# Kernel optimization log

Hardware: AMD Instinct MI355X
Metric: run time of the kernel (lower is better)

The kernel has to match this reference:

```python
import jax, jax.numpy as jnp
import numpy as np

VOC = 32000
D = 512          # embedding_dim == hidden_dim
POS = 1024       # position_embeddings_count


def _layernorm(x, gamma, beta, eps=1e-5):
    mu = jnp.mean(x, axis=-1, keepdims=True)
    var = jnp.var(x, axis=-1, keepdims=True)
    return (x - mu) * jax.lax.rsqrt(var + eps) * gamma + beta


def setup_inputs() -> dict:
    key = jax.random.key(0)
    ks = jax.random.split(key, 7)
    inp = jax.random.randint(ks[0], (32, 1024), 0, VOC)
    word_emb = jax.random.normal(ks[1], (VOC, D), dtype=jnp.float32) * 0.02
    pos_emb = jax.random.normal(ks[2], (POS, D), dtype=jnp.float32) * 0.02
    gamma = jnp.ones((D,), dtype=jnp.float32)
    beta = jnp.zeros((D,), dtype=jnp.float32)
    # torch.rand -> uniform [0,1) init in the original Attention module
    Wk = jax.random.uniform(ks[3], (D, D), dtype=jnp.float32)
    Wq = jax.random.uniform(ks[4], (D, D), dtype=jnp.float32)
    Wv = jax.random.uniform(ks[5], (D, D), dtype=jnp.float32)
    return {"input": inp, "word_emb": word_emb, "pos_emb": pos_emb,
            "gamma": gamma, "beta": beta, "Wk": Wk, "Wq": Wq, "Wv": Wv}


def reference(input, word_emb, pos_emb, gamma, beta, Wk, Wq, Wv):
    S = input.shape[-1]
    # MiniBertEmbedding: word + positional, then LayerNorm
    emb = word_emb[input] + pos_emb[:S][None, :, :]   # [B,S,D]
    x = _layernorm(emb, gamma, beta)
    # Attention: single-head QK^T softmax V with param matrices
    k = jnp.einsum('bsd,dh->bsh', x, Wk)
    q = jnp.einsum('bsd,dh->bsh', x, Wq)
    v = jnp.einsum('bsd,do->bso', x, Wv)
    qk = jnp.einsum('bqh,bkh->bqk', q, k) / jnp.sqrt(jnp.float32(D))
    attn = jax.nn.softmax(qk, axis=-1)
    return jnp.einsum('bqk,bko->bqo', attn, v)
```

## Files before the change

kernel.cpp:

```cpp
#include <hip/hip_runtime.h>
#include <math.h>

typedef _Float16 f16;
typedef _Float16 half8 __attribute__((ext_vector_type(8)));
typedef _Float16 hv2 __attribute__((ext_vector_type(2)));
typedef _Float16 hv4 __attribute__((ext_vector_type(4)));
typedef float f32x4 __attribute__((ext_vector_type(4)));
typedef __attribute__((address_space(1))) const unsigned int gu32;
typedef __attribute__((address_space(3))) unsigned int lu32;

#define BB 32
#define SS 1024
#define DD 512
#define NR (BB*SS)
#define CH 16

__device__ __forceinline__ void stage128(const char* g, int ldb, char* lds,
                                         int wv, int ln) {
  #pragma unroll
  for (int r = 0; r < 4; r++) {
    int slot = r * 256 + wv * 64 + ln;
    int row = slot >> 3, cp = slot & 7;
    int c = cp ^ (row & 7);
    const char* gp = g + (size_t)row * ldb + (c << 4);
    char* lp = lds + ((slot - ln) << 4);
    __builtin_amdgcn_global_load_lds((gu32*)gp, (lu32*)lp, 16, 0, 0);
  }
}

__device__ __forceinline__ void stage8k_512(const char* g, int ldb, char* lds) {
  int tid = threadIdx.x;
  int slot = tid;
  int row = slot >> 3, cp = slot & 7;
  int c = cp ^ (row & 7);
  const char* gp = g + (size_t)row * ldb + (c << 4);
  char* lp = lds + ((slot - (tid & 63)) << 4);
  __builtin_amdgcn_global_load_lds((gu32*)gp, (lu32*)lp, 16, 0, 0);
}

__device__ __forceinline__ half8 frag_ld(const char* lds, int row, int kc) {
  return *(const half8*)(lds + row * 128 + ((kc ^ (row & 7)) << 4));
}

__device__ __forceinline__ f32x4 MF(half8 a, half8 b, f32x4 c) {
  return __builtin_amdgcn_mfma_f32_16x16x32_f16(a, b, c, 0, 0, 0);
}

__global__ __launch_bounds__(256) void k_prep(
    const int* __restrict__ inp, const float* __restrict__ wemb,
    const float* __restrict__ pemb, const float* __restrict__ gamma,
    const float* __restrict__ beta, f16* __restrict__ Xhi, f16* __restrict__ Xlo,
    const float* __restrict__ Wq, const float* __restrict__ Wk,
    const float* __restrict__ Wv, f16* __restrict__ Wqh, f16* __restrict__ Wql,
    f16* __restrict__ Wkh, f16* __restrict__ Wkl, f16* __restrict__ Wvt)
{
  int bid = blockIdx.x;
  int tid = threadIdx.x;
  __shared__ float red[10];
  __shared__ float Lt[64][65];
  if (bid >= NR) {
    int t  = bid - NR;
    int mz = t >> 6;
    int tt = t & 63;
    if (mz < 2) {
      const float* W = mz ? Wk : Wq;
      f16* Oh = mz ? Wkh : Wqh;
      f16* Ol = mz ? Wkl : Wql;
      #pragma unroll
      for (int p = 0; p < 4; p++) {
        size_t base = (size_t)tt * 4096 + p * 1024 + tid * 4;
        float4 v = *(const float4*)&W[base];
        f16 h0 = (f16)v.x, h1 = (f16)v.y, h2 = (f16)v.z, h3 = (f16)v.w;
        hv4 hi = {h0, h1, h2, h3};
        hv4 lo = {(f16)(v.x - (float)h0), (f16)(v.y - (float)h1),
                  (f16)(v.z - (float)h2), (f16)(v.w - (float)h3)};
        *(hv4*)&Oh[base] = hi;
        *(hv4*)&Ol[base] = lo;
      }
      return;
    }
    int tr = tt >> 3, tc = tt & 7;
    int rr = tid >> 4;
    int c4 = (tid & 15) * 4;
    #pragma unroll
    for (int p = 0; p < 4; p++) {
      float4 v = *(const float4*)&Wv[(size_t)(tr * 64 + p * 16 + rr) * DD + tc * 64 + c4];
      Lt[p * 16 + rr][c4 + 0] = v.x; Lt[p * 16 + rr][c4 + 1] = v.y;
      Lt[p * 16 + rr][c4 + 2] = v.z; Lt[p * 16 + rr][c4 + 3] = v.w;
    }
    __syncthreads();
    #pragma unroll
    for (int p = 0; p < 4; p++) {
      int dl = p * 16 + rr;
      float v0 = Lt[c4 + 0][dl], v1 = Lt[c4 + 1][dl];
      float v2 = Lt[c4 + 2][dl], v3 = Lt[c4 + 3][dl];
      size_t o = (size_t)(tc * 64 + dl) * DD + tr * 64 + c4;
      *(hv4*)&Wvt[o] = (hv4){(f16)v0, (f16)v1, (f16)v2, (f16)v3};
    }
    return;
  }
  int row = bid;
  int s   = row & (SS - 1);
  int tok = inp[row];
  float2 w = ((const float2*)(wemb + (size_t)tok * DD))[tid];
  float2 p = ((const float2*)(pemb + (size_t)s   * DD))[tid];
  float ex = w.x + p.x, ey = w.y + p.y;
  float sum = ex + ey, ssq = ex*ex + ey*ey;
  #pragma unroll
  for (int off = 32; off > 0; off >>= 1) {
    sum += __shfl_down(sum, off, 64);
    ssq += __shfl_down(ssq, off, 64);
  }
  int wv = tid >> 6, ln = tid & 63;
  if (ln == 0) { red[wv] = sum; red[4 + wv] = ssq; }
  __syncthreads();
  if (tid == 0) {
    float s4 = red[0] + red[1] + red[2] + red[3];
    float q4 = red[4] + red[5] + red[6] + red[7];
    float mean = s4 * (1.0f / DD);
    float var  = q4 * (1.0f / DD) - mean * mean;
    red[8] = mean; red[9] = rsqrtf(var + 1e-5f);
  }
  __syncthreads();
  float mean = red[8], rstd = red[9];
  float2 g  = ((const float2*)gamma)[tid];
  float2 bt = ((const float2*)beta)[tid];
  float ox = (ex - mean) * rstd * g.x + bt.x;
  float oy = (ey - mean) * rstd * g.y + bt.y;
  f16 hx = (f16)ox, hy = (f16)oy;
  f16 lx = (f16)(ox - (float)hx), ly = (f16)(oy - (float)hy);
  ((hv2*)(Xhi + (size_t)row * DD))[tid] = (hv2){hx, hy};
  ((hv2*)(Xlo + (size_t)row * DD))[tid] = (hv2){lx, ly};
}

__global__ __launch_bounds__(256, 2) void k_mt(
    const f16* __restrict__ Wkh, const f16* __restrict__ Wkl,
    const f16* __restrict__ Wqh, const f16* __restrict__ Wql,
    f16* __restrict__ Mthi, f16* __restrict__ Mtlo)
{
  __shared__ __align__(16) char Ah[16384], Al[16384], Bh[16384], Bl[16384];
  int tid = threadIdx.x, wv = tid >> 6, ln = tid & 63;
  int mw = wv & 1, nw = wv >> 1;
  int n0 = blockIdx.x * 128;
  int m0 = blockIdx.y * 128;
  f32x4 acc[4][4];
  #pragma unroll
  for (int i = 0; i < 4; i++)
    #pragma unroll
    for (int j = 0; j < 4; j++) acc[i][j] = (f32x4)(0.0f);
  int quad = ln >> 4, l15 = ln & 15;
  for (int k0 = 0; k0 < DD; k0 += 64) {
    __syncthreads();
    stage128((const char*)(Wkh + (size_t)m0 * DD + k0), 1024, Ah, wv, ln);
    stage128((const char*)(Wkl + (size_t)m0 * DD + k0), 1024, Al, wv, ln);
    stage128((const char*)(Wqh + (size_t)n0 * DD + k0), 1024, Bh, wv, ln);
    stage128((const char*)(Wql + (size_t)n0 * DD + k0), 1024, Bl, wv, ln);
    __syncthreads();
    #pragma unroll
    for (int ks = 0; ks < 2; ks++) {
      int kc = ks * 4 + quad;
      half8 ah[4], al[4], bh[4], bl[4];
      #pragma unroll
      for (int t = 0; t < 4; t++) {
        ah[t] = frag_ld(Ah, mw * 64 + t * 16 + l15, kc);
        al[t] = frag_ld(Al, mw * 64 + t * 16 + l15, kc);
        bh[t] = frag_ld(Bh, nw * 64 + t * 16 + l15, kc);
        bl[t] = frag_ld(Bl, nw * 64 + t * 16 + l15, kc);
      }
      #pragma unroll
      for (int i = 0; i < 4; i++)
        #pragma unroll
        for (int j = 0; j < 4; j++) {
          acc[i][j] = MF(ah[i], bh[j], acc[i][j]);
          acc[i][j] = MF(ah[i], bl[j], acc[i][j]);
          acc[i][j] = MF(al[i], bh[j], acc[i][j]);
        }
    }
  }
  #pragma unroll
  for (int i = 0; i < 4; i++)
    #pragma unroll
    for (int j = 0; j < 4; j++)
      #pragma unroll
      for (int rg = 0; rg < 4; rg++) {
        int gm = m0 + mw * 64 + i * 16 + quad * 4 + rg;
        int gn = n0 + nw * 64 + j * 16 + l15;
        size_t o = (size_t)gm * DD + gn;
        float v = acc[i][j][rg];
        f16 h = (f16)v;
        Mthi[o] = h; Mtlo[o] = (f16)(v - (float)h);
      }
}

__global__ __launch_bounds__(256, 2) void k_projm(
    const f16* __restrict__ Xhi, const f16* __restrict__ Xlo,
    const f16* __restrict__ Mthi, const f16* __restrict__ Mtlo,
    f16* __restrict__ Sqhi, f16* __restrict__ Sqlo)
{
  __shared__ __align__(16) char Ah[16384], Al[16384], Bh[16384], Bl[16384];
  int tid = threadIdx.x, wv = tid >> 6, ln = tid & 63;
  int mw = wv & 1, nw = wv >> 1;
  int L = blockIdx.x;
  int xb = (L >> 3) & 3;
  int y  = ((L >> 5) << 3) + (L & 7);
  int n0 = xb * 128;
  int m0 = y * 128;
  f32x4 acc[4][4];
  #pragma unroll
  for (int i = 0; i < 4; i++)
    #pragma unroll
    for (int j = 0; j < 4; j++) acc[i][j] = (f32x4)(0.0f);
  int quad = ln >> 4, l15 = ln & 15;
  for (int k0 = 0; k0 < DD; k0 += 64) {
    __syncthreads();
    stage128((const char*)(Xhi  + (size_t)m0 * DD + k0), 1024, Ah, wv, ln);
    stage128((const char*)(Xlo  + (size_t)m0 * DD + k0), 1024, Al, wv, ln);
    stage128((const char*)(Mthi + (size_t)n0 * DD + k0), 1024, Bh, wv, ln);
    stage128((const char*)(Mtlo + (size_t)n0 * DD + k0), 1024, Bl, wv, ln);
    __syncthreads();
    #pragma unroll
    for (int ks = 0; ks < 2; ks++) {
      int kc = ks * 4 + quad;
      half8 ah[4], al[4], bh[4], bl[4];
      #pragma unroll
      for (int t = 0; t < 4; t++) {
        ah[t] = frag_ld(Ah, mw * 64 + t * 16 + l15, kc);
        al[t] = frag_ld(Al, mw * 64 + t * 16 + l15, kc);
        bh[t] = frag_ld(Bh, nw * 64 + t * 16 + l15, kc);
        bl[t] = frag_ld(Bl, nw * 64 + t * 16 + l15, kc);
      }
      #pragma unroll
      for (int i = 0; i < 4; i++)
        #pragma unroll
        for (int j = 0; j < 4; j++) {
          acc[i][j] = MF(ah[i], bh[j], acc[i][j]);
          acc[i][j] = MF(ah[i], bl[j], acc[i][j]);
          acc[i][j] = MF(al[i], bh[j], acc[i][j]);
        }
    }
  }
  #pragma unroll
  for (int i = 0; i < 4; i++)
    #pragma unroll
    for (int j = 0; j < 4; j++)
      #pragma unroll
      for (int rg = 0; rg < 4; rg++) {
        int gm = m0 + mw * 64 + i * 16 + quad * 4 + rg;
        int gn = n0 + nw * 64 + j * 16 + l15;
        size_t o = (size_t)gm * DD + gn;
        float v = acc[i][j][rg];
        f16 h = (f16)v;
        Sqhi[o] = h; Sqlo[o] = (f16)(v - (float)h);
      }
}

__global__ __launch_bounds__(256, 2) void k_vt(
    const f16* __restrict__ Wvt, const f16* __restrict__ Xhi, f16* __restrict__ Vt)
{
  __shared__ __align__(16) char Ah[2][16384], Bh[2][16384];
  int tid = threadIdx.x, wv = tid >> 6, ln = tid & 63;
  int mw = wv & 1, nw = wv >> 1;
  int orig = blockIdx.x;
  int L = (orig & 7) * 128 + (orig >> 3);
  int c = L >> 7, t = L & 127;
  int m0 = (t & 3) * 128;
  int n0 = (c * 32 + (t >> 2)) * 128;
  f32x4 acc[4][4];
  #pragma unroll
  for (int i = 0; i < 4; i++)
    #pragma unroll
    for (int j = 0; j < 4; j++) acc[i][j] = (f32x4)(0.0f);
  int quad = ln >> 4, l15 = ln & 15;
  stage128((const char*)(Wvt + (size_t)m0 * DD), 1024, Ah[0], wv, ln);
  stage128((const char*)(Xhi + (size_t)n0 * DD), 1024, Bh[0], wv, ln);
  for (int k0 = 0; k0 < DD; k0 += 64) {
    int cur = (k0 >> 6) & 1;
    __builtin_amdgcn_s_barrier();
    __builtin_amdgcn_sched_barrier(0);
    if (k0 + 64 < DD) {
      stage128((const char*)(Wvt + (size_t)m0 * DD + k0 + 64), 1024, Ah[cur ^ 1], wv, ln);
      stage128((const char*)(Xhi + (size_t)n0 * DD + k0 + 64), 1024, Bh[cur ^ 1], wv, ln);
      asm volatile("s_waitcnt vmcnt(8)" ::: "memory");
    } else {
      asm volatile("s_waitcnt vmcnt(0)" ::: "memory");
    }
    __builtin_amdgcn_s_barrier();
    __builtin_amdgcn_sched_barrier(0);
    #pragma unroll
    for (int ks = 0; ks < 2; ks++) {
      int kc = ks * 4 + quad;
      half8 a[4], b[4];
      #pragma unroll
      for (int tt = 0; tt < 4; tt++) {
        a[tt] = frag_ld(Ah[cur], mw * 64 + tt * 16 + l15, kc);
        b[tt] = frag_ld(Bh[cur], nw * 64 + tt * 16 + l15, kc);
      }
      #pragma unroll
      for (int i = 0; i < 4; i++)
        #pragma unroll
        for (int j = 0; j < 4; j++) acc[i][j] = MF(a[i], b[j], acc[i][j]);
    }
  }
  #pragma unroll
  for (int i = 0; i < 4; i++)
    #pragma unroll
    for (int j = 0; j < 4; j++)
      #pragma unroll
      for (int rg = 0; rg < 4; rg++) {
        int gm = m0 + mw * 64 + i * 16 + quad * 4 + rg;
        int gn = n0 + nw * 64 + j * 16 + l15;
        Vt[(size_t)gm * NR + gn] = (f16)acc[i][j][rg];
      }
}

__global__ __launch_bounds__(512, 2) void k_qk(
    const f16* __restrict__ Sqhi, const f16* __restrict__ Sqlo,
    const f16* __restrict__ Xhi, const f16* __restrict__ Xlo,
    f16* __restrict__ Pws, f16* __restrict__ Pd)
{
  __shared__ __align__(16) char Ah[8192], Al[8192];
  __shared__ __align__(16) char Bh[2][4][8192], Bl[2][4][8192];
  __shared__ float redm[4][64], reds[4][64];
  int tid = threadIdx.x, wv = tid >> 6, ln = tid & 63;
  int rowg = wv & 1, qd = wv >> 1;
  int L = blockIdx.x;
  int g  = L >> 7;
  int rr = L & 127;
  int z  = g * 8 + (rr & 7);
  int m0 = (rr >> 3) * 64;
  size_t zr = (size_t)z * SS;
  f32x4 acc[2][16];
  #pragma unroll
  for (int i = 0; i < 2; i++)
    #pragma unroll
    for (int j = 0; j < 16; j++) acc[i][j] = (f32x4)(0.0f);
  int quad = ln >> 4, l15 = ln & 15;

  #pragma unroll
  for (int q4 = 0; q4 < 4; q4++) {
    stage8k_512((const char*)(Xhi + (zr + q4 * 256) * DD), 1024, Bh[0][q4]);
    stage8k_512((const char*)(Xlo + (zr + q4 * 256) * DD), 1024, Bl[0][q4]);
  }

  half8 afh[2][2], afl[2][2];
  for (int k0 = 0; k0 < DD; k0 += 64) {
    #pragma unroll
    for (int r = 0; r < 4; r++) {
      __builtin_amdgcn_s_barrier();
      __builtin_amdgcn_sched_barrier(0);
      if (r == 0) {
        stage8k_512((const char*)(Sqhi + (zr + m0) * DD + k0), 1024, Ah);
        stage8k_512((const char*)(Sqlo + (zr + m0) * DD + k0), 1024, Al);
      }
      bool haveNext = !(k0 == DD - 64 && r == 3);
      if (haveNext) {
        int nk0 = (r == 3) ? k0 + 64 : k0;
        int nr  = (r + 1) & 3;
        #pragma unroll
        for (int q4 = 0; q4 < 4; q4++) {
          int n0 = q4 * 256 + nr * 64;
          stage8k_512((const char*)(Xhi + (zr + n0) * DD + nk0), 1024, Bh[(r + 1) & 1][q4]);
          stage8k_512((const char*)(Xlo + (zr + n0) * DD + nk0), 1024, Bl[(r + 1) & 1][q4]);
        }
        asm volatile("s_waitcnt vmcnt(8)" ::: "memory");
      } else {
        asm volatile("s_waitcnt vmcnt(0)" ::: "memory");
      }
      __builtin_amdgcn_s_barrier();
      __builtin_amdgcn_sched_barrier(0);
      if (r == 0) {
        #pragma unroll
        for (int ks = 0; ks < 2; ks++)
          #pragma unroll
          for (int i = 0; i < 2; i++) {
            afh[ks][i] = frag_ld(Ah, rowg * 32 + i * 16 + l15, ks * 4 + quad);
            afl[ks][i] = frag_ld(Al, rowg * 32 + i * 16 + l15, ks * 4 + quad);
          }
      }
      #pragma unroll
      for (int ks = 0; ks < 2; ks++) {
        int kc = ks * 4 + quad;
        #pragma unroll
        for (int jj = 0; jj < 4; jj++) {
          half8 bh = frag_ld(Bh[r & 1][qd], jj * 16 + l15, kc);
          half8 bl = frag_ld(Bl[r & 1][qd], jj * 16 + l15, kc);
          #pragma unroll
          for (int i = 0; i < 2; i++) {
            acc[i][r * 4 + jj] = MF(afh[ks][i], bh, acc[i][r * 4 + jj]);
            acc[i][r * 4 + jj] = MF(afh[ks][i], bl, acc[i][r * 4 + jj]);
            acc[i][r * 4 + jj] = MF(afl[ks][i], bh, acc[i][r * 4 + jj]);
          }
        }
      }
    }
  }

  const float scale = 0.044194173824159216f;
  float mx[2][4];
  #pragma unroll
  for (int i = 0; i < 2; i++)
    #pragma unroll
    for (int rg = 0; rg < 4; rg++) mx[i][rg] = -3.0e38f;
  #pragma unroll
  for (int i = 0; i < 2; i++)
    #pragma unroll
    for (int j = 0; j < 16; j++)
      #pragma unroll
      for (int rg = 0; rg < 4; rg++) {
        acc[i][j][rg] *= scale;
        mx[i][rg] = fmaxf(mx[i][rg], acc[i][j][rg]);
      }
  #pragma unroll
  for (int off = 1; off < 16; off <<= 1)
    #pragma unroll
    for (int i = 0; i < 2; i++)
      #pragma unroll
      for (int rg = 0; rg < 4; rg++)
        mx[i][rg] = fmaxf(mx[i][rg], __shfl_xor(mx[i][rg], off, 64));
  if (l15 == 0) {
    #pragma unroll
    for (int i = 0; i < 2; i++)
      #pragma unroll
      for (int rg = 0; rg < 4; rg++)
        redm[qd][rowg * 32 + i * 16 + quad * 4 + rg] = mx[i][rg];
  }
  __syncthreads();
  float fm[2][4], sum[2][4];
  #pragma unroll
  for (int i = 0; i < 2; i++)
    #pragma unroll
    for (int rg = 0; rg < 4; rg++) {
      int row = rowg * 32 + i * 16 + quad * 4 + rg;
      fm[i][rg] = fmaxf(fmaxf(redm[0][row], redm[1][row]),
                        fmaxf(redm[2][row], redm[3][row]));
      sum[i][rg] = 0.0f;
    }
  #pragma unroll
  for (int i = 0; i < 2; i++)
    #pragma unroll
    for (int j = 0; j < 16; j++)
      #pragma unroll
      for (int rg = 0; rg < 4; rg++) {
        float e = __expf(acc[i][j][rg] - fm[i][rg]);
        acc[i][j][rg] = e;
        sum[i][rg] += e;
      }
  #pragma unroll
  for (int off = 1; off < 16; off <<= 1)
    #pragma unroll
    for (int i = 0; i < 2; i++)
      #pragma unroll
      for (int rg = 0; rg < 4; rg++)
        sum[i][rg] += __shfl_xor(sum[i][rg], off, 64);
  if (l15 == 0) {
    #pragma unroll
    for (int i = 0; i < 2; i++)
      #pragma unroll
      for (int rg = 0; rg < 4; rg++)
        reds[qd][rowg * 32 + i * 16 + quad * 4 + rg] = sum[i][rg];
  }
  __syncthreads();
  float inv[2][4];
  #pragma unroll
  for (int i = 0; i < 2; i++)
    #pragma unroll
    for (int rg = 0; rg < 4; rg++) {
      int row = rowg * 32 + i * 16 + quad * 4 + rg;
      inv[i][rg] = 1.0f / (reds[0][row] + reds[1][row] + reds[2][row] + reds[3][row]);
    }
  f16* Pb = (z < CH) ? Pws : Pd;
  size_t zo = (size_t)((z < CH) ? z : z - CH);
  #pragma unroll
  for (int i = 0; i < 2; i++)
    #pragma unroll
    for (int j = 0; j < 16; j++)
      #pragma unroll
      for (int rg = 0; rg < 4; rg++) {
        int row = rowg * 32 + i * 16 + quad * 4 + rg;
        int col = qd * 256 + j * 16 + l15;
        Pb[(zo * SS + m0 + row) * SS + col] = (f16)(acc[i][j][rg] * inv[i][rg]);
      }
}

__global__ __launch_bounds__(256, 2) void k_pv(
    const f16* __restrict__ P, const f16* __restrict__ Vt, float* __restrict__ O,
    int zoff)
{
  __shared__ __align__(16) char Ah[2][16384], Bh[2][16384];
  int tid = threadIdx.x, wv = tid >> 6, ln = tid & 63;
  int mw = wv & 1, nw = wv >> 1;
  int orig = blockIdx.x;
  int L = (orig & 7) * 64 + (orig >> 3);
  int c = L >> 6, t = L & 63;
  int zl = 2 * c + (t >> 5);
  int m0 = ((t >> 2) & 7) * 128;
  int n0 = (t & 3) * 128;
  int b  = zoff + zl;
  const char* Pt = (const char*)(P + ((size_t)zl * SS + m0) * SS);
  const char* Vb = (const char*)(Vt + (size_t)n0 * NR + (size_t)b * SS);
  f32x4 acc[4][4];
  #pragma unroll
  for (int i = 0; i < 4; i++)
    #pragma unroll
    for (int j = 0; j < 4; j++) acc[i][j] = (f32x4)(0.0f);
  int quad = ln >> 4, l15 = ln & 15;
  stage128(Pt, 2048, Ah[0], wv, ln);
  stage128(Vb, NR * 2, Bh[0], wv, ln);
  for (int k0 = 0; k0 < SS; k0 += 64) {
    int cur = (k0 >> 6) & 1;
    __builtin_amdgcn_s_barrier();
    __builtin_amdgcn_sched_barrier(0);
    if (k0 + 64 < SS) {
      stage128(Pt + (k0 + 64) * 2, 2048, Ah[cur ^ 1], wv, ln);
      stage128(Vb + (k0 + 64) * 2, NR * 2, Bh[cur ^ 1], wv, ln);
      asm volatile("s_waitcnt vmcnt(8)" ::: "memory");
    } else {
      asm volatile("s_waitcnt vmcnt(0)" ::: "memory");
    }
    __builtin_amdgcn_s_barrier();
    __builtin_amdgcn_sched_barrier(0);
    #pragma unroll
    for (int ks = 0; ks < 2; ks++) {
      int kc = ks * 4 + quad;
      half8 a[4], bf[4];
      #pragma unroll
      for (int tt = 0; tt < 4; tt++) {
        a[tt]  = frag_ld(Ah[cur], mw * 64 + tt * 16 + l15, kc);
        bf[tt] = frag_ld(Bh[cur], nw * 64 + tt * 16 + l15, kc);
      }
      #pragma unroll
      for (int i = 0; i < 4; i++)
        #pragma unroll
        for (int j = 0; j < 4; j++) acc[i][j] = MF(a[i], bf[j], acc[i][j]);
    }
  }
  #pragma unroll
  for (int i = 0; i < 4; i++)
    #pragma unroll
    for (int j = 0; j < 4; j++)
      #pragma unroll
      for (int rg = 0; rg < 4; rg++) {
        int gm = m0 + mw * 64 + i * 16 + quad * 4 + rg;
        int gn = n0 + nw * 64 + j * 16 + l15;
        O[((size_t)b * SS + gm) * DD + gn] = acc[i][j][rg];
      }
}

extern "C" void kernel_launch(void* const* d_in, const int* in_sizes, int n_in,
                              void* d_out, int out_size, void* d_ws, size_t ws_size,
                              hipStream_t stream) {
  const int*   inp   = (const int*)d_in[0];
  const float* wemb  = (const float*)d_in[1];
  const float* pemb  = (const float*)d_in[2];
  const float* gamma = (const float*)d_in[3];
  const float* beta  = (const float*)d_in[4];
  const float* Wk    = (const float*)d_in[5];
  const float* Wq    = (const float*)d_in[6];
  const float* Wv    = (const float*)d_in[7];

  char* ws = (char*)d_ws;
  f16* Xhi  = (f16*)ws;
  f16* Xlo  = (f16*)(ws + ((size_t)32 << 20));
  f16* Sqhi = (f16*)(ws + ((size_t)64 << 20));
  f16* Sqlo = (f16*)(ws + ((size_t)96 << 20));
  f16* Vt   = (f16*)(ws + ((size_t)128 << 20));
  f16* Pws  = (f16*)(ws + ((size_t)160 << 20));
  f16* Pd   = (f16*)d_out;

  f16* Wqh  = (f16*)d_out;
  f16* Wql  = Wqh + (size_t)DD * DD;
  f16* Wkh  = Wql + (size_t)DD * DD;
  f16* Wkl  = Wkh + (size_t)DD * DD;
  f16* Wvt  = Wkl + (size_t)DD * DD;
  f16* Mthi = Wvt + (size_t)DD * DD;
  f16* Mtlo = Mthi + (size_t)DD * DD;

  k_prep<<<NR + 192, 256, 0, stream>>>(inp, wemb, pemb, gamma, beta, Xhi, Xlo,
                                       Wq, Wk, Wv, Wqh, Wql, Wkh, Wkl, Wvt);
  k_mt<<<dim3(DD / 128, DD / 128), 256, 0, stream>>>(Wkh, Wkl, Wqh, Wql, Mthi, Mtlo);
  k_projm<<<1024, 256, 0, stream>>>(Xhi, Xlo, Mthi, Mtlo, Sqhi, Sqlo);
  k_vt<<<1024, 256, 0, stream>>>(Wvt, Xhi, Vt);
  k_qk<<<512, 512, 0, stream>>>(Sqhi, Sqlo, Xhi, Xlo, Pws, Pd);
  k_pv<<<512, 256, 0, stream>>>(Pd,  Vt, (float*)d_out, CH);
  k_pv<<<512, 256, 0, stream>>>(Pws, Vt, (float*)d_out, 0);
}
```

Before: 425.1 us.

## Widen projm to 8 waves, load Q fragments directly, and raise MFMA priority in qk

k_projm now runs with 512 threads per block, giving each wave a 64x32 output tile instead of 64x64. This cuts accumulator registers per wave and doubles the waves available to hide latency. In k_qk the A-operand Sq fragments are read straight from global memory into registers, dropping two LDS staging buffers and their loads, and the MFMA section is wrapped in s_setprio. The direct global loads are uncoalesced and sit before a barrier, which may add latency, and the freed LDS may raise occupancy.

```diff
diff --git a/kernel.cpp b/kernel.cpp
--- a/kernel.cpp
+++ b/kernel.cpp
@@ -36,6 +36,19 @@
   const char* gp = g + (size_t)row * ldb + (c << 4);
   char* lp = lds + ((slot - (tid & 63)) << 4);
   __builtin_amdgcn_global_load_lds((gu32*)gp, (lu32*)lp, 16, 0, 0);
+}
+
+__device__ __forceinline__ void stage16k_512(const char* g, int ldb, char* lds) {
+  int tid = threadIdx.x;
+  #pragma unroll
+  for (int r = 0; r < 2; r++) {
+    int slot = r * 512 + tid;
+    int row = slot >> 3, cp = slot & 7;
+    int c = cp ^ (row & 7);
+    const char* gp = g + (size_t)row * ldb + (c << 4);
+    char* lp = lds + ((slot - (tid & 63)) << 4);
+    __builtin_amdgcn_global_load_lds((gu32*)gp, (lu32*)lp, 16, 0, 0);
+  }
 }
 
 __device__ __forceinline__ half8 frag_ld(const char* lds, int row, int kc) {
@@ -192,7 +205,7 @@
       }
 }
 
-__global__ __launch_bounds__(256, 2) void k_projm(
+__global__ __launch_bounds__(512, 4) void k_projm(
     const f16* __restrict__ Xhi, const f16* __restrict__ Xlo,
     const f16* __restrict__ Mthi, const f16* __restrict__ Mtlo,
     f16* __restrict__ Sqhi, f16* __restrict__ Sqlo)
@@ -205,34 +218,37 @@
   int y  = ((L >> 5) << 3) + (L & 7);
   int n0 = xb * 128;
   int m0 = y * 128;
-  f32x4 acc[4][4];
-  #pragma unroll
-  for (int i = 0; i < 4; i++)
-    #pragma unroll
-    for (int j = 0; j < 4; j++) acc[i][j] = (f32x4)(0.0f);
+  f32x4 acc[4][2];
+  #pragma unroll
+  for (int i = 0; i < 4; i++)
+    #pragma unroll
+    for (int j = 0; j < 2; j++) acc[i][j] = (f32x4)(0.0f);
   int quad = ln >> 4, l15 = ln & 15;
   for (int k0 = 0; k0 < DD; k0 += 64) {
     __syncthreads();
-    stage128((const char*)(Xhi  + (size_t)m0 * DD + k0), 1024, Ah, wv, ln);
-    stage128((const char*)(Xlo  + (size_t)m0 * DD + k0), 1024, Al, wv, ln);
-    stage128((const char*)(Mthi + (size_t)n0 * DD + k0), 1024, Bh, wv, ln);
-    stage128((const char*)(Mtlo + (size_t)n0 * DD + k0), 1024, Bl, wv, ln);
+    stage16k_512((const char*)(Xhi  + (size_t)m0 * DD + k0), 1024, Ah);
+    stage16k_512((const char*)(Xlo  + (size_t)m0 * DD + k0), 1024, Al);
+    stage16k_512((const char*)(Mthi + (size_t)n0 * DD + k0), 1024, Bh);
+    stage16k_512((const char*)(Mtlo + (size_t)n0 * DD + k0), 1024, Bl);
     __syncthreads();
     #pragma unroll
     for (int ks = 0; ks < 2; ks++) {
       int kc = ks * 4 + quad;
-      half8 ah[4], al[4], bh[4], bl[4];
+      half8 ah[4], al[4], bh[2], bl[2];
       #pragma unroll
       for (int t = 0; t < 4; t++) {
         ah[t] = frag_ld(Ah, mw * 64 + t * 16 + l15, kc);
         al[t] = frag_ld(Al, mw * 64 + t * 16 + l15, kc);
-        bh[t] = frag_ld(Bh, nw * 64 + t * 16 + l15, kc);
-        bl[t] = frag_ld(Bl, nw * 64 + t * 16 + l15, kc);
+      }
+      #pragma unroll
+      for (int t = 0; t < 2; t++) {
+        bh[t] = frag_ld(Bh, nw * 32 + t * 16 + l15, kc);
+        bl[t] = frag_ld(Bl, nw * 32 + t * 16 + l15, kc);
       }
       #pragma unroll
       for (int i = 0; i < 4; i++)
         #pragma unroll
-        for (int j = 0; j < 4; j++) {
+        for (int j = 0; j < 2; j++) {
           acc[i][j] = MF(ah[i], bh[j], acc[i][j]);
           acc[i][j] = MF(ah[i], bl[j], acc[i][j]);
           acc[i][j] = MF(al[i], bh[j], acc[i][j]);
@@ -242,11 +258,11 @@
   #pragma unroll
   for (int i = 0; i < 4; i++)
     #pragma unroll
-    for (int j = 0; j < 4; j++)
+    for (int j = 0; j < 2; j++)
       #pragma unroll
       for (int rg = 0; rg < 4; rg++) {
         int gm = m0 + mw * 64 + i * 16 + quad * 4 + rg;
-        int gn = n0 + nw * 64 + j * 16 + l15;
+        int gn = n0 + nw * 32 + j * 16 + l15;
         size_t o = (size_t)gm * DD + gn;
         float v = acc[i][j][rg];
         f16 h = (f16)v;
@@ -318,7 +334,6 @@
     const f16* __restrict__ Xhi, const f16* __restrict__ Xlo,
     f16* __restrict__ Pws, f16* __restrict__ Pd)
 {
-  __shared__ __align__(16) char Ah[8192], Al[8192];
   __shared__ __align__(16) char Bh[2][4][8192], Bl[2][4][8192];
   __shared__ float redm[4][64], reds[4][64];
   int tid = threadIdx.x, wv = tid >> 6, ln = tid & 63;
@@ -349,8 +364,14 @@
       __builtin_amdgcn_s_barrier();
       __builtin_amdgcn_sched_barrier(0);
       if (r == 0) {
-        stage8k_512((const char*)(Sqhi + (zr + m0) * DD + k0), 1024, Ah);
-        stage8k_512((const char*)(Sqlo + (zr + m0) * DD + k0), 1024, Al);
+        #pragma unroll
+        for (int ks = 0; ks < 2; ks++)
+          #pragma unroll
+          for (int i = 0; i < 2; i++) {
+            int row = rowg * 32 + i * 16 + l15;
+            afh[ks][i] = *(const half8*)(Sqhi + (zr + m0 + row) * DD + k0 + (ks * 4 + quad) * 8);
+            afl[ks][i] = *(const half8*)(Sqlo + (zr + m0 + row) * DD + k0 + (ks * 4 + quad) * 8);
+          }
       }
       bool haveNext = !(k0 == DD - 64 && r == 3);
       if (haveNext) {
@@ -368,15 +389,7 @@
       }
       __builtin_amdgcn_s_barrier();
       __builtin_amdgcn_sched_barrier(0);
-      if (r == 0) {
-        #pragma unroll
-        for (int ks = 0; ks < 2; ks++)
-          #pragma unroll
-          for (int i = 0; i < 2; i++) {
-            afh[ks][i] = frag_ld(Ah, rowg * 32 + i * 16 + l15, ks * 4 + quad);
-            afl[ks][i] = frag_ld(Al, rowg * 32 + i * 16 + l15, ks * 4 + quad);
-          }
-      }
+      __builtin_amdgcn_s_setprio(1);
       #pragma unroll
       for (int ks = 0; ks < 2; ks++) {
         int kc = ks * 4 + quad;
@@ -392,6 +405,7 @@
           }
         }
       }
+      __builtin_amdgcn_s_setprio(0);
     }
   }
 
@@ -578,7 +592,7 @@
   k_prep<<<NR + 192, 256, 0, stream>>>(inp, wemb, pemb, gamma, beta, Xhi, Xlo,
                                        Wq, Wk, Wv, Wqh, Wql, Wkh, Wkl, Wvt);
   k_mt<<<dim3(DD / 128, DD / 128), 256, 0, stream>>>(Wkh, Wkl, Wqh, Wql, Mthi, Mtlo);
-  k_projm<<<1024, 256, 0, stream>>>(Xhi, Xlo, Mthi, Mtlo, Sqhi, Sqlo);
+  k_projm<<<1024, 512, 0, stream>>>(Xhi, Xlo, Mthi, Mtlo, Sqhi, Sqlo);
   k_vt<<<1024, 256, 0, stream>>>(Wvt, Xhi, Vt);
   k_qk<<<512, 512, 0, stream>>>(Sqhi, Sqlo, Xhi, Xlo, Pws, Pd);
   k_pv<<<512, 256, 0, stream>>>(Pd,  Vt, (float*)d_out, CH);
```

After: 450.4 us. 6.0% more time.

## Merge projection and V-transpose GEMMs into one launch; prefetch Sq tiles in QK

Applied to the files above, without the earlier changes.

Combines the k_projm and k_vt kernels into a single 2048-block launch that branches on block index and shares one 64KB LDS buffer. This removes a kernel launch boundary and lets the two independent GEMMs' blocks run concurrently, filling tail gaps. In k_qk, the Sq hi/lo tiles for the next k-slice are now prefetched during the previous phase instead of loaded synchronously at r==0, with waitcnt adjusted. The shared LDS footprint (64KB) may limit occupancy for the V-transpose path, which previously used the same size.

```diff
diff --git a/kernel.cpp b/kernel.cpp
--- a/kernel.cpp
+++ b/kernel.cpp
@@ -192,125 +192,128 @@
       }
 }
 
-__global__ __launch_bounds__(256, 2) void k_projm(
+__global__ __launch_bounds__(256, 2) void k_pjvt(
     const f16* __restrict__ Xhi, const f16* __restrict__ Xlo,
     const f16* __restrict__ Mthi, const f16* __restrict__ Mtlo,
-    f16* __restrict__ Sqhi, f16* __restrict__ Sqlo)
+    f16* __restrict__ Sqhi, f16* __restrict__ Sqlo,
+    const f16* __restrict__ Wvt, f16* __restrict__ Vt)
 {
-  __shared__ __align__(16) char Ah[16384], Al[16384], Bh[16384], Bl[16384];
+  __shared__ __align__(16) char Lds[65536];
+  int bid = blockIdx.x;
   int tid = threadIdx.x, wv = tid >> 6, ln = tid & 63;
-  int mw = wv & 1, nw = wv >> 1;
-  int L = blockIdx.x;
-  int xb = (L >> 3) & 3;
-  int y  = ((L >> 5) << 3) + (L & 7);
-  int n0 = xb * 128;
-  int m0 = y * 128;
-  f32x4 acc[4][4];
-  #pragma unroll
-  for (int i = 0; i < 4; i++)
-    #pragma unroll
-    for (int j = 0; j < 4; j++) acc[i][j] = (f32x4)(0.0f);
   int quad = ln >> 4, l15 = ln & 15;
-  for (int k0 = 0; k0 < DD; k0 += 64) {
-    __syncthreads();
-    stage128((const char*)(Xhi  + (size_t)m0 * DD + k0), 1024, Ah, wv, ln);
-    stage128((const char*)(Xlo  + (size_t)m0 * DD + k0), 1024, Al, wv, ln);
-    stage128((const char*)(Mthi + (size_t)n0 * DD + k0), 1024, Bh, wv, ln);
-    stage128((const char*)(Mtlo + (size_t)n0 * DD + k0), 1024, Bl, wv, ln);
-    __syncthreads();
-    #pragma unroll
-    for (int ks = 0; ks < 2; ks++) {
-      int kc = ks * 4 + quad;
-      half8 ah[4], al[4], bh[4], bl[4];
-      #pragma unroll
-      for (int t = 0; t < 4; t++) {
-        ah[t] = frag_ld(Ah, mw * 64 + t * 16 + l15, kc);
-        al[t] = frag_ld(Al, mw * 64 + t * 16 + l15, kc);
-        bh[t] = frag_ld(Bh, nw * 64 + t * 16 + l15, kc);
-        bl[t] = frag_ld(Bl, nw * 64 + t * 16 + l15, kc);
-      }
-      #pragma unroll
-      for (int i = 0; i < 4; i++)
-        #pragma unroll
-        for (int j = 0; j < 4; j++) {
-          acc[i][j] = MF(ah[i], bh[j], acc[i][j]);
-          acc[i][j] = MF(ah[i], bl[j], acc[i][j]);
-          acc[i][j] = MF(al[i], bh[j], acc[i][j]);
-        }
-    }
-  }
-  #pragma unroll
-  for (int i = 0; i < 4; i++)
-    #pragma unroll
-    for (int j = 0; j < 4; j++)
-      #pragma unroll
-      for (int rg = 0; rg < 4; rg++) {
-        int gm = m0 + mw * 64 + i * 16 + quad * 4 + rg;
-        int gn = n0 + nw * 64 + j * 16 + l15;
-        size_t o = (size_t)gm * DD + gn;
-        float v = acc[i][j][rg];
-        f16 h = (f16)v;
-        Sqhi[o] = h; Sqlo[o] = (f16)(v - (float)h);
-      }
-}
-
-__global__ __launch_bounds__(256, 2) void k_vt(
-    const f16* __restrict__ Wvt, const f16* __restrict__ Xhi, f16* __restrict__ Vt)
-{
-  __shared__ __align__(16) char Ah[2][16384], Bh[2][16384];
-  int tid = threadIdx.x, wv = tid >> 6, ln = tid & 63;
-  int mw = wv & 1, nw = wv >> 1;
-  int orig = blockIdx.x;
-  int L = (orig & 7) * 128 + (orig >> 3);
-  int c = L >> 7, t = L & 127;
-  int m0 = (t & 3) * 128;
-  int n0 = (c * 32 + (t >> 2)) * 128;
-  f32x4 acc[4][4];
-  #pragma unroll
-  for (int i = 0; i < 4; i++)
-    #pragma unroll
-    for (int j = 0; j < 4; j++) acc[i][j] = (f32x4)(0.0f);
-  int quad = ln >> 4, l15 = ln & 15;
-  stage128((const char*)(Wvt + (size_t)m0 * DD), 1024, Ah[0], wv, ln);
-  stage128((const char*)(Xhi + (size_t)n0 * DD), 1024, Bh[0], wv, ln);
-  for (int k0 = 0; k0 < DD; k0 += 64) {
-    int cur = (k0 >> 6) & 1;
-    __builtin_amdgcn_s_barrier();
-    __builtin_amdgcn_sched_barrier(0);
-    if (k0 + 64 < DD) {
-      stage128((const char*)(Wvt + (size_t)m0 * DD + k0 + 64), 1024, Ah[cur ^ 1], wv, ln);
-      stage128((const char*)(Xhi + (size_t)n0 * DD + k0 + 64), 1024, Bh[cur ^ 1], wv, ln);
-      asm volatile("s_waitcnt vmcnt(8)" ::: "memory");
-    } else {
-      asm volatile("s_waitcnt vmcnt(0)" ::: "memory");
-    }
-    __builtin_amdgcn_s_barrier();
-    __builtin_amdgcn_sched_barrier(0);
-    #pragma unroll
-    for (int ks = 0; ks < 2; ks++) {
-      int kc = ks * 4 + quad;
-      half8 a[4], b[4];
-      #pragma unroll
-      for (int tt = 0; tt < 4; tt++) {
-        a[tt] = frag_ld(Ah[cur], mw * 64 + tt * 16 + l15, kc);
-        b[tt] = frag_ld(Bh[cur], nw * 64 + tt * 16 + l15, kc);
-      }
-      #pragma unroll
-      for (int i = 0; i < 4; i++)
-        #pragma unroll
-        for (int j = 0; j < 4; j++) acc[i][j] = MF(a[i], b[j], acc[i][j]);
-    }
-  }
-  #pragma unroll
-  for (int i = 0; i < 4; i++)
-    #pragma unroll
-    for (int j = 0; j < 4; j++)
-      #pragma unroll
-      for (int rg = 0; rg < 4; rg++) {
-        int gm = m0 + mw * 64 + i * 16 + quad * 4 + rg;
-        int gn = n0 + nw * 64 + j * 16 + l15;
-        Vt[(size_t)gm * NR + gn] = (f16)acc[i][j][rg];
-      }
+  if (bid < 1024) {
+    char* Ah = Lds;           char* Al = Lds + 16384;
+    char* Bh = Lds + 32768;   char* Bl = Lds + 49152;
+    int mw = wv & 1, nw = wv >> 1;
+    int L = bid;
+    int xb = (L >> 3) & 3;
+    int y  = ((L >> 5) << 3) + (L & 7);
+    int n0 = xb * 128;
+    int m0 = y * 128;
+    f32x4 acc[4][4];
+    #pragma unroll
+    for (int i = 0; i < 4; i++)
+      #pragma unroll
+      for (int j = 0; j < 4; j++) acc[i][j] = (f32x4)(0.0f);
+    for (int k0 = 0; k0 < DD; k0 += 64) {
+      __syncthreads();
+      stage128((const char*)(Xhi  + (size_t)m0 * DD + k0), 1024, Ah, wv, ln);
+      stage128((const char*)(Xlo  + (size_t)m0 * DD + k0), 1024, Al, wv, ln);
+      stage128((const char*)(Mthi + (size_t)n0 * DD + k0), 1024, Bh, wv, ln);
+      stage128((const char*)(Mtlo + (size_t)n0 * DD + k0), 1024, Bl, wv, ln);
+      __syncthreads();
+      #pragma unroll
+      for (int ks = 0; ks < 2; ks++) {
+        int kc = ks * 4 + quad;
+        half8 ah[4], al[4], bh[4], bl[4];
+        #pragma unroll
+        for (int t = 0; t < 4; t++) {
+          ah[t] = frag_ld(Ah, mw * 64 + t * 16 + l15, kc);
+          al[t] = frag_ld(Al, mw * 64 + t * 16 + l15, kc);
+          bh[t] = frag_ld(Bh, nw * 64 + t * 16 + l15, kc);
+          bl[t] = frag_ld(Bl, nw * 64 + t * 16 + l15, kc);
+        }
+        #pragma unroll
+        for (int i = 0; i < 4; i++)
+          #pragma unroll
+          for (int j = 0; j < 4; j++) {
+            acc[i][j] = MF(ah[i], bh[j], acc[i][j]);
+            acc[i][j] = MF(ah[i], bl[j], acc[i][j]);
+            acc[i][j] = MF(al[i], bh[j], acc[i][j]);
+          }
+      }
+    }
+    #pragma unroll
+    for (int i = 0; i < 4; i++)
+      #pragma unroll
+      for (int j = 0; j < 4; j++)
+        #pragma unroll
+        for (int rg = 0; rg < 4; rg++) {
+          int gm = m0 + mw * 64 + i * 16 + quad * 4 + rg;
+          int gn = n0 + nw * 64 + j * 16 + l15;
+          size_t o = (size_t)gm * DD + gn;
+          float v = acc[i][j][rg];
+          f16 h = (f16)v;
+          Sqhi[o] = h; Sqlo[o] = (f16)(v - (float)h);
+        }
+  } else {
+    int mw = wv & 1, nw = wv >> 1;
+    int orig = bid - 1024;
+    int L = (orig & 7) * 128 + (orig >> 3);
+    int c = L >> 7, t = L & 127;
+    int m0 = (t & 3) * 128;
+    int n0 = (c * 32 + (t >> 2)) * 128;
+    f32x4 acc[4][4];
+    #pragma unroll
+    for (int i = 0; i < 4; i++)
+      #pragma unroll
+      for (int j = 0; j < 4; j++) acc[i][j] = (f32x4)(0.0f);
+    stage128((const char*)(Wvt + (size_t)m0 * DD), 1024, Lds, wv, ln);
+    stage128((const char*)(Xhi + (size_t)n0 * DD), 1024, Lds + 32768, wv, ln);
+    for (int k0 = 0; k0 < DD; k0 += 64) {
+      int cur = (k0 >> 6) & 1;
+      char* Ac = Lds + cur * 16384;
+      char* Bc = Lds + 32768 + cur * 16384;
+      __builtin_amdgcn_s_barrier();
+      __builtin_amdgcn_sched_barrier(0);
+      if (k0 + 64 < DD) {
+        stage128((const char*)(Wvt + (size_t)m0 * DD + k0 + 64), 1024,
+                 Lds + (cur ^ 1) * 16384, wv, ln);
+        stage128((const char*)(Xhi + (size_t)n0 * DD + k0 + 64), 1024,
+                 Lds + 32768 + (cur ^ 1) * 16384, wv, ln);
+        asm volatile("s_waitcnt vmcnt(8)" ::: "memory");
+      } else {
+        asm volatile("s_waitcnt vmcnt(0)" ::: "memory");
+      }
+      __builtin_amdgcn_s_barrier();
+      __builtin_amdgcn_sched_barrier(0);
+      #pragma unroll
+      for (int ks = 0; ks < 2; ks++) {
+        int kc = ks * 4 + quad;
+        half8 a[4], b[4];
+        #pragma unroll
+        for (int tt = 0; tt < 4; tt++) {
+          a[tt] = frag_ld(Ac, mw * 64 + tt * 16 + l15, kc);
+          b[tt] = frag_ld(Bc, nw * 64 + tt * 16 + l15, kc);
+        }
+        #pragma unroll
+        for (int i = 0; i < 4; i++)
+          #pragma unroll
+          for (int j = 0; j < 4; j++) acc[i][j] = MF(a[i], b[j], acc[i][j]);
+      }
+    }
+    #pragma unroll
+    for (int i = 0; i < 4; i++)
+      #pragma unroll
+      for (int j = 0; j < 4; j++)
+        #pragma unroll
+        for (int rg = 0; rg < 4; rg++) {
+          int gm = m0 + mw * 64 + i * 16 + quad * 4 + rg;
+          int gn = n0 + nw * 64 + j * 16 + l15;
+          Vt[(size_t)gm * NR + gn] = (f16)acc[i][j][rg];
+        }
+  }
 }
 
 __global__ __launch_bounds__(512, 2) void k_qk(
@@ -336,6 +339,8 @@
     for (int j = 0; j < 16; j++) acc[i][j] = (f32x4)(0.0f);
   int quad = ln >> 4, l15 = ln & 15;
 
+  stage8k_512((const char*)(Sqhi + (zr + m0) * DD), 1024, Ah);
+  stage8k_512((const char*)(Sqlo + (zr + m0) * DD), 1024, Al);
   #pragma unroll
   for (int q4 = 0; q4 < 4; q4++) {
     stage8k_512((const char*)(Xhi + (zr + q4 * 256) * DD), 1024, Bh[0][q4]);
@@ -348,12 +353,8 @@
     for (int r = 0; r < 4; r++) {
       __builtin_amdgcn_s_barrier();
       __builtin_amdgcn_sched_barrier(0);
-      if (r == 0) {
-        stage8k_512((const char*)(Sqhi + (zr + m0) * DD + k0), 1024, Ah);
-        stage8k_512((const char*)(Sqlo + (zr + m0) * DD + k0), 1024, Al);
-      }
-      bool haveNext = !(k0 == DD - 64 && r == 3);
-      if (haveNext) {
+      bool lastPhase = (k0 == DD - 64 && r == 3);
+      if (!lastPhase) {
         int nk0 = (r == 3) ? k0 + 64 : k0;
         int nr  = (r + 1) & 3;
         #pragma unroll
@@ -362,7 +363,13 @@
           stage8k_512((const char*)(Xhi + (zr + n0) * DD + nk0), 1024, Bh[(r + 1) & 1][q4]);
           stage8k_512((const char*)(Xlo + (zr + n0) * DD + nk0), 1024, Bl[(r + 1) & 1][q4]);
         }
-        asm volatile("s_waitcnt vmcnt(8)" ::: "memory");
+        if (r == 3) {
+          stage8k_512((const char*)(Sqhi + (zr + m0) * DD + k0 + 64), 1024, Ah);
+          stage8k_512((const char*)(Sqlo + (zr + m0) * DD + k0 + 64), 1024, Al);
+          asm volatile("s_waitcnt vmcnt(10)" ::: "memory");
+        } else {
+          asm volatile("s_waitcnt vmcnt(8)" ::: "memory");
+        }
       } else {
         asm volatile("s_waitcnt vmcnt(0)" ::: "memory");
       }
@@ -578,8 +585,7 @@
   k_prep<<<NR + 192, 256, 0, stream>>>(inp, wemb, pemb, gamma, beta, Xhi, Xlo,
                                        Wq, Wk, Wv, Wqh, Wql, Wkh, Wkl, Wvt);
   k_mt<<<dim3(DD / 128, DD / 128), 256, 0, stream>>>(Wkh, Wkl, Wqh, Wql, Mthi, Mtlo);
-  k_projm<<<1024, 256, 0, stream>>>(Xhi, Xlo, Mthi, Mtlo, Sqhi, Sqlo);
-  k_vt<<<1024, 256, 0, stream>>>(Wvt, Xhi, Vt);
+  k_pjvt<<<2048, 256, 0, stream>>>(Xhi, Xlo, Mthi, Mtlo, Sqhi, Sqlo, Wvt, Vt);
   k_qk<<<512, 512, 0, stream>>>(Sqhi, Sqlo, Xhi, Xlo, Pws, Pd);
   k_pv<<<512, 256, 0, stream>>>(Pd,  Vt, (float*)d_out, CH);
   k_pv<<<512, 256, 0, stream>>>(Pws, Vt, (float*)d_out, 0);
```

New measurement: 393.1 us. 1.08x faster.
